# Optimization experiments

Measured on AMD Instinct MI355X. Metric: run time of the kernel, lower is better.

The kernel has to match this reference:

```python
import jax, jax.numpy as jnp
import numpy as np

H = 16      # numHeads (== numKeyValueHeads since keyValueHeadsPerHead=1)
D = 128     # headDim


def setup_inputs() -> dict:
    key = jax.random.key(0)
    k1, k2, k3 = jax.random.split(key, 3)
    B, S, dim = 2, 2048, 2048
    x = jax.random.normal(k1, (B, S, dim), dtype=jnp.float32)
    # qkvProj: Linear(dim -> (H + 2*H)*D) without bias; torch Linear weight is [out, in]
    Wqkv = jax.random.normal(k2, ((H + 2 * H) * D, dim), dtype=jnp.float32) * 0.02
    # outProj: Linear(H*D -> dim) without bias
    Wout = jax.random.normal(k3, (dim, H * D), dtype=jnp.float32) * 0.02
    return {"x": x, "Wqkv": Wqkv, "Wout": Wout}


def reference(x, Wqkv, Wout):
    B, S, _ = x.shape
    qkv = jnp.einsum('bsd,ed->bse', x, Wqkv)           # [B, S, 3*H*D]
    qkv = qkv.reshape(B, S, 3 * H, D)
    q = qkv[:, :, :H]                                  # [B, S, H, D]
    k = qkv[:, :, H:2 * H]                             # [B, S, H, D]
    v = qkv[:, :, 2 * H:]                              # [B, S, H, D]
    # explicit QK^T / sqrt(d), softmax in fp32, then @ V (keyValueHeadsPerHead=1
    # collapses the group axis, leaving standard per-head attention)
    logits = jnp.einsum('bqhd,bkhd->bhqk', q, k) * (D ** -0.5)
    w = jax.nn.softmax(logits.astype(jnp.float32), axis=-1).astype(logits.dtype)
    out = jnp.einsum('bhqk,bkhd->bqhd', w, v).reshape(B, S, H * D)
    return jnp.einsum('bse,de->bsd', out, Wout)        # outProj
```

## Files before the change

kernel.cpp:

```cpp
#include <hip/hip_runtime.h>

typedef __bf16 bf16x8 __attribute__((ext_vector_type(8)));
typedef _Float16 f16;
typedef f16 f16x8 __attribute__((ext_vector_type(8)));
typedef float f32x4 __attribute__((ext_vector_type(4)));
typedef unsigned short u16;
typedef u16 u16x4 __attribute__((ext_vector_type(4)));

__device__ __forceinline__ u16 f2bf(float f) {
  unsigned u = __builtin_bit_cast(unsigned, f);
  u += 0x7FFFu + ((u >> 16) & 1u);
  return (u16)(u >> 16);
}

#define GLDS16(g, l) __builtin_amdgcn_global_load_lds(                     \
    (const __attribute__((address_space(1))) unsigned int*)(g),            \
    (__attribute__((address_space(3))) unsigned int*)(l), 16, 0, 0)

__device__ __forceinline__ f32x4 mfma16(bf16x8 a, bf16x8 b, f32x4 c) {
  return __builtin_amdgcn_mfma_f32_16x16x32_bf16(a, b, c, 0, 0, 0);
}
__device__ __forceinline__ f32x4 mfma16h(f16x8 a, f16x8 b, f32x4 c) {
  return __builtin_amdgcn_mfma_f32_16x16x32_f16(a, b, c, 0, 0, 0);
}

__global__ void cvt_all(const float* __restrict__ x, const float* __restrict__ wqkv,
                        const float* __restrict__ wout, u16* __restrict__ xb,
                        u16* __restrict__ wqkvb, u16* __restrict__ woutb, float qscale) {
  int idx = blockIdx.x * blockDim.x + threadIdx.x;
  int stride = gridDim.x * blockDim.x;
  for (int i = idx; i < 6291456; i += stride) {
    const float* src; u16* dst; int j; float sc = 1.0f;
    if (i < 2097152)      { src = x;    dst = xb;    j = i; }
    else if (i < 5242880) { j = i - 2097152; src = wqkv; dst = wqkvb;
                            if (j < 1048576) sc = qscale; }
    else                  { j = i - 5242880; src = wout; dst = woutb; }
    float4 v = ((const float4*)src)[j];
    u16x4 o = { f2bf(v.x * sc), f2bf(v.y * sc), f2bf(v.z * sc), f2bf(v.w * sc) };
    ((u16x4*)dst)[j] = o;
  }
}

__global__ __launch_bounds__(512, 1) void gemm1_qkv(
    const u16* __restrict__ A, const u16* __restrict__ B,
    u16* __restrict__ QK, u16* __restrict__ VT) {
  __shared__ __align__(16) u16 LA[2][16384];
  __shared__ __align__(16) u16 LB[2][16384];
  constexpr int K = 2048;
  const int t = threadIdx.x, lane = t & 63, w = t >> 6;
  const int wm = w >> 2, wn = w & 3;
  const int l15 = lane & 15, lg = lane >> 4;
  const int l7 = l15 & 7;

  const int bid = blockIdx.x;
  const int wg = (bid & 7) * 48 + (bid >> 3);
  const int bx = wg % 24, by = wg / 24;
  const int m0 = by * 256, n0 = bx * 256;

  const int srow = t >> 3;
  const int schunk = (t & 7) ^ (srow & 7);
  const u16* ga = A + (size_t)(m0 + srow) * K + schunk * 8;
  const u16* gb = B + (size_t)(n0 + srow) * K + schunk * 8;

  f32x4 acc[8][4] = {};

#define SA(c, kt, d) GLDS16(ga + (kt) * 64 + (size_t)(c) * 64 * K, &LA[d][(c) * 4096] + t * 8)
#define SB(c, kt, d) GLDS16(gb + (kt) * 64 + (size_t)(c) * 64 * K, &LB[d][(c) * 4096] + t * 8)
#define BAR() __builtin_amdgcn_s_barrier()
#define LGKM0() asm volatile("s_waitcnt lgkmcnt(0)" ::: "memory")

  SA(0, 0, 0); SA(2, 0, 0); SB(0, 0, 0); SB(1, 0, 0); SB(2, 0, 0); SB(3, 0, 0);
  SA(1, 0, 0); SA(3, 0, 0);
  SA(0, 1, 1); SA(2, 1, 1); SB(0, 1, 1); SB(1, 1, 1); SB(2, 1, 1); SB(3, 1, 1);
  asm volatile("s_waitcnt vmcnt(6)" ::: "memory");
  BAR();

#pragma unroll 1
  for (int T = 0; T < 16; ++T) {
    const int k0 = 2 * T, k1 = 2 * T + 1;
    const bool st = (T < 15);
    bf16x8 aLo[2][4], aHi[2][4], bLo[2][2], bHi[2][2];

#pragma unroll
    for (int kk = 0; kk < 2; ++kk) {
      const int cp = ((kk * 4 + lg) ^ l7) * 8;
#pragma unroll
      for (int i = 0; i < 4; ++i)
        aLo[kk][i] = *(const bf16x8*)&LA[0][(wm * 128 + i * 16 + l15) * 64 + cp];
#pragma unroll
      for (int j = 0; j < 2; ++j)
        bLo[kk][j] = *(const bf16x8*)&LB[0][(wn * 64 + j * 16 + l15) * 64 + cp];
    }
    SA(1, k1, 1); SA(3, k1, 1);
    asm volatile("s_waitcnt lgkmcnt(8)" ::: "memory");
    BAR(); LGKM0();
    __builtin_amdgcn_s_setprio(1);
#pragma unroll
    for (int i = 0; i < 4; ++i)
#pragma unroll
      for (int j = 0; j < 2; ++j)
#pragma unroll
        for (int kk = 0; kk < 2; ++kk)
          acc[i][j] = mfma16(aLo[kk][i], bLo[kk][j], acc[i][j]);
    __builtin_amdgcn_s_setprio(0);
    BAR();

#pragma unroll
    for (int kk = 0; kk < 2; ++kk) {
      const int cp = ((kk * 4 + lg) ^ l7) * 8;
#pragma unroll
      for (int j = 0; j < 2; ++j)
        bHi[kk][j] = *(const bf16x8*)&LB[0][(wn * 64 + 32 + j * 16 + l15) * 64 + cp];
    }
    if (st) { SA(0, k0 + 2, 0); SA(2, k0 + 2, 0); }
    BAR(); LGKM0();
    __builtin_amdgcn_s_setprio(1);
#pragma unroll
    for (int i = 0; i < 4; ++i)
#pragma unroll
      for (int j = 0; j < 2; ++j)
#pragma unroll
        for (int kk = 0; kk < 2; ++kk)
          acc[i][2 + j] = mfma16(aLo[kk][i], bHi[kk][j], acc[i][2 + j]);
    __builtin_amdgcn_s_setprio(0);
    BAR();

#pragma unroll
    for (int kk = 0; kk < 2; ++kk) {
      const int cp = ((kk * 4 + lg) ^ l7) * 8;
#pragma unroll
      for (int i = 0; i < 4; ++i)
        aHi[kk][i] = *(const bf16x8*)&LA[0][(wm * 128 + 64 + i * 16 + l15) * 64 + cp];
    }
    if (st) { SB(0, k0 + 2, 0); SB(1, k0 + 2, 0); }
    BAR(); LGKM0();
    __builtin_amdgcn_s_setprio(1);
#pragma unroll
    for (int i = 0; i < 4; ++i)
#pragma unroll
      for (int j = 0; j < 2; ++j)
#pragma unroll
        for (int kk = 0; kk < 2; ++kk)
          acc[4 + i][j] = mfma16(aHi[kk][i], bLo[kk][j], acc[4 + i][j]);
    __builtin_amdgcn_s_setprio(0);
    BAR();

    if (st) {
      SB(2, k0 + 2, 0); SB(3, k0 + 2, 0);
      asm volatile("s_waitcnt vmcnt(6)" ::: "memory");
    } else {
      asm volatile("s_waitcnt vmcnt(0)" ::: "memory");
    }
    BAR();
    __builtin_amdgcn_s_setprio(1);
#pragma unroll
    for (int i = 0; i < 4; ++i)
#pragma unroll
      for (int j = 0; j < 2; ++j)
#pragma unroll
        for (int kk = 0; kk < 2; ++kk)
          acc[4 + i][2 + j] = mfma16(aHi[kk][i], bHi[kk][j], acc[4 + i][2 + j]);
    __builtin_amdgcn_s_setprio(0);
    BAR();

#pragma unroll
    for (int kk = 0; kk < 2; ++kk) {
      const int cp = ((kk * 4 + lg) ^ l7) * 8;
#pragma unroll
      for (int i = 0; i < 4; ++i)
        aLo[kk][i] = *(const bf16x8*)&LA[1][(wm * 128 + i * 16 + l15) * 64 + cp];
#pragma unroll
      for (int j = 0; j < 2; ++j)
        bLo[kk][j] = *(const bf16x8*)&LB[1][(wn * 64 + j * 16 + l15) * 64 + cp];
    }
    if (st) { SA(1, k0 + 2, 0); SA(3, k0 + 2, 0); }
    asm volatile("s_waitcnt lgkmcnt(8)" ::: "memory");
    BAR(); LGKM0();
    __builtin_amdgcn_s_setprio(1);
#pragma unroll
    for (int i = 0; i < 4; ++i)
#pragma unroll
      for (int j = 0; j < 2; ++j)
#pragma unroll
        for (int kk = 0; kk < 2; ++kk)
          acc[i][j] = mfma16(aLo[kk][i], bLo[kk][j], acc[i][j]);
    __builtin_amdgcn_s_setprio(0);
    BAR();

#pragma unroll
    for (int kk = 0; kk < 2; ++kk) {
      const int cp = ((kk * 4 + lg) ^ l7) * 8;
#pragma unroll
      for (int j = 0; j < 2; ++j)
        bHi[kk][j] = *(const bf16x8*)&LB[1][(wn * 64 + 32 + j * 16 + l15) * 64 + cp];
    }
    if (st) { SA(0, k1 + 2, 1); SA(2, k1 + 2, 1); }
    BAR(); LGKM0();
    __builtin_amdgcn_s_setprio(1);
#pragma unroll
    for (int i = 0; i < 4; ++i)
#pragma unroll
      for (int j = 0; j < 2; ++j)
#pragma unroll
        for (int kk = 0; kk < 2; ++kk)
          acc[i][2 + j] = mfma16(aLo[kk][i], bHi[kk][j], acc[i][2 + j]);
    __builtin_amdgcn_s_setprio(0);
    BAR();

#pragma unroll
    for (int kk = 0; kk < 2; ++kk) {
      const int cp = ((kk * 4 + lg) ^ l7) * 8;
#pragma unroll
      for (int i = 0; i < 4; ++i)
        aHi[kk][i] = *(const bf16x8*)&LA[1][(wm * 128 + 64 + i * 16 + l15) * 64 + cp];
    }
    if (st) { SB(0, k1 + 2, 1); SB(1, k1 + 2, 1); }
    BAR(); LGKM0();
    __builtin_amdgcn_s_setprio(1);
#pragma unroll
    for (int i = 0; i < 4; ++i)
#pragma unroll
      for (int j = 0; j < 2; ++j)
#pragma unroll
        for (int kk = 0; kk < 2; ++kk)
          acc[4 + i][j] = mfma16(aHi[kk][i], bLo[kk][j], acc[4 + i][j]);
    __builtin_amdgcn_s_setprio(0);
    BAR();

    if (st) {
      SB(2, k1 + 2, 1); SB(3, k1 + 2, 1);
      asm volatile("s_waitcnt vmcnt(6)" ::: "memory");
    }
    BAR();
    __builtin_amdgcn_s_setprio(1);
#pragma unroll
    for (int i = 0; i < 4; ++i)
#pragma unroll
      for (int j = 0; j < 2; ++j)
#pragma unroll
        for (int kk = 0; kk < 2; ++kk)
          acc[4 + i][2 + j] = mfma16(aHi[kk][i], bHi[kk][j], acc[4 + i][2 + j]);
    __builtin_amdgcn_s_setprio(0);
    BAR();
  }
#undef SA
#undef SB
#undef BAR
#undef LGKM0

  const int rb = m0 + wm * 128 + lg * 4;
  const int cb0 = wn * 64 + l15;
  if (n0 < 4096) {
#pragma unroll
    for (int i = 0; i < 8; ++i)
#pragma unroll
      for (int j = 0; j < 4; ++j) {
        const int row0 = rb + i * 16;
        const int col = n0 + cb0 + j * 16;
#pragma unroll
        for (int jj = 0; jj < 4; ++jj)
          QK[(size_t)(row0 + jj) * 4096 + col] = f2bf(acc[i][j][jj]);
      }
  } else {
#pragma unroll
    for (int i = 0; i < 8; ++i)
#pragma unroll
      for (int j = 0; j < 4; ++j) {
        const int row0 = rb + i * 16;
        const int vcol = (n0 - 4096) + cb0 + j * 16;
        const int bb = row0 >> 11, s = row0 & 2047;
        auto h0 = __builtin_amdgcn_cvt_pkrtz(acc[i][j][0], acc[i][j][1]);
        auto h1 = __builtin_amdgcn_cvt_pkrtz(acc[i][j][2], acc[i][j][3]);
        uint2 pk;
        pk.x = __builtin_bit_cast(unsigned, h0);
        pk.y = __builtin_bit_cast(unsigned, h1);
        *(uint2*)&VT[((size_t)bb * 2048 + vcol) * 2048 + s] = pk;
      }
  }
}

__global__ __launch_bounds__(256, 2) void gemm2_out(
    const u16* __restrict__ A, const u16* __restrict__ B,
    float* __restrict__ C) {
  __shared__ __align__(16) u16 LA[2][8192];
  __shared__ __align__(16) u16 LB[2][8192];
  constexpr int K = 2048, N = 2048;
  const int t = threadIdx.x, lane = t & 63, w = t >> 6;
  const int wm = w >> 1, wn = w & 1;
  const int l15 = lane & 15, lg = lane >> 4;
  const int l7 = l15 & 7;

  const int bid = blockIdx.x;
  const int wg = (bid & 7) * 64 + (bid >> 3);
  const int bx = wg & 15, by = wg >> 4;
  const int m0 = by * 128, n0 = bx * 128;

  const int srow = t >> 3;
  const int schunk = (t & 7) ^ (srow & 7);
  const u16* ga = A + (size_t)(m0 + srow) * K + schunk * 8;
  const u16* gb = B + (size_t)(n0 + srow) * K + schunk * 8;

  f32x4 acc[4][4] = {};

#define STG_A(ch, kt, bfi)                                                 \
    GLDS16(ga + (kt) * 64 + (size_t)(ch) * 32 * K, &LA[bfi][(ch) * 2048] + t * 8)
#define STG_B(ch, kt, bfi)                                                 \
    GLDS16(gb + (kt) * 64 + (size_t)(ch) * 32 * K, &LB[bfi][(ch) * 2048] + t * 8)
#define STG_ALL(kt, bfi) do {                                              \
    STG_A(0, kt, bfi); STG_A(1, kt, bfi); STG_A(2, kt, bfi); STG_A(3, kt, bfi); \
    STG_B(0, kt, bfi); STG_B(1, kt, bfi); STG_B(2, kt, bfi); STG_B(3, kt, bfi); \
  } while (0)

  STG_ALL(0, 0);

#pragma unroll 1
  for (int T = 0; T < 32; ++T) {
    const int p = T & 1, np = p ^ 1;
    if (T < 31) {
      STG_ALL(T + 1, np);
      asm volatile("s_waitcnt vmcnt(8)" ::: "memory");
    } else {
      asm volatile("s_waitcnt vmcnt(0)" ::: "memory");
    }
    __builtin_amdgcn_s_barrier();

    const u16* la = &LA[p][0];
    const u16* lb = &LB[p][0];
    bf16x8 aLo[2][2], aHi[2][2], bLo[2][2], bHi[2][2];
#pragma unroll
    for (int kk = 0; kk < 2; ++kk) {
      const int cp = ((kk * 4 + lg) ^ l7) * 8;
#pragma unroll
      for (int i = 0; i < 2; ++i) {
        aLo[kk][i] = *(const bf16x8*)&la[(wm * 64 + i * 16 + l15) * 64 + cp];
        bLo[kk][i] = *(const bf16x8*)&lb[(wn * 64 + i * 16 + l15) * 64 + cp];
        bHi[kk][i] = *(const bf16x8*)&lb[(wn * 64 + 32 + i * 16 + l15) * 64 + cp];
        aHi[kk][i] = *(const bf16x8*)&la[(wm * 64 + 32 + i * 16 + l15) * 64 + cp];
      }
    }
#pragma unroll
    for (int i = 0; i < 2; ++i)
#pragma unroll
      for (int j = 0; j < 2; ++j)
#pragma unroll
        for (int kk = 0; kk < 2; ++kk)
          acc[i][j] = mfma16(aLo[kk][i], bLo[kk][j], acc[i][j]);
#pragma unroll
    for (int i = 0; i < 2; ++i)
#pragma unroll
      for (int j = 0; j < 2; ++j)
#pragma unroll
        for (int kk = 0; kk < 2; ++kk)
          acc[i][2 + j] = mfma16(aLo[kk][i], bHi[kk][j], acc[i][2 + j]);
#pragma unroll
    for (int i = 0; i < 2; ++i)
#pragma unroll
      for (int j = 0; j < 2; ++j)
#pragma unroll
        for (int kk = 0; kk < 2; ++kk)
          acc[2 + i][j] = mfma16(aHi[kk][i], bLo[kk][j], acc[2 + i][j]);
#pragma unroll
    for (int i = 0; i < 2; ++i)
#pragma unroll
      for (int j = 0; j < 2; ++j)
#pragma unroll
        for (int kk = 0; kk < 2; ++kk)
          acc[2 + i][2 + j] = mfma16(aHi[kk][i], bHi[kk][j], acc[2 + i][2 + j]);

    asm volatile("s_waitcnt lgkmcnt(0)" ::: "memory");
    __builtin_amdgcn_s_barrier();
  }
#undef STG_A
#undef STG_B
#undef STG_ALL

  const int rb = m0 + wm * 64 + lg * 4;
  const int cb = n0 + wn * 64 + l15;
#pragma unroll
  for (int i = 0; i < 4; ++i)
#pragma unroll
    for (int j = 0; j < 4; ++j) {
      const int row0 = rb + i * 16;
      const int col = cb + j * 16;
#pragma unroll
      for (int jj = 0; jj < 4; ++jj)
        C[(size_t)(row0 + jj) * N + col] = acc[i][j][jj];
    }
}

#define PSTRIDE 72
__global__ __launch_bounds__(512, 1) void attn_fwd(
    const u16* __restrict__ qk, const u16* __restrict__ vt, u16* __restrict__ aout) {
  __shared__ __align__(16) u16 Ks[2][64 * 128];
  __shared__ __align__(16) u16 Vs[2][128 * 64];
  __shared__ __align__(16) u16 Pl[8][32 * PSTRIDE];
  const int t = threadIdx.x, lane = t & 63, w = t >> 6;
  const int bh = blockIdx.x;
  const int b = bh >> 4, h = bh & 15;
  const int q0 = blockIdx.y * 256 + w * 32;
  const int l15 = lane & 15, lg = lane >> 4;

  const u16* qp = qk + (size_t)b * 2048 * 4096 + h * 128;
  const u16* kp = qp + 2048;
  const u16* vtp = vt + (size_t)(b * 16 + h) * 128 * 2048;
  u16* op = aout + (size_t)b * 2048 * 2048 + h * 128;

  int ksoff[2], vsoff[2];
#pragma unroll
  for (int rd = 0; rd < 2; ++rd) {
    const int r = rd * 32 + (t >> 4);
    const int c = (t & 15) ^ (r & 15);
    ksoff[rd] = r * 4096 + c * 8;
    const int rv = rd * 64 + (t >> 3);
    const int cv = (t & 7) ^ (rv & 7);
    vsoff[rd] = rv * 2048 + cv * 8;
  }

  bf16x8 qf[2][4];
#pragma unroll
  for (int mi = 0; mi < 2; ++mi)
#pragma unroll
    for (int kd = 0; kd < 4; ++kd)
      qf[mi][kd] = *(const bf16x8*)&qp[(size_t)(q0 + mi * 16 + l15) * 4096 + kd * 32 + lg * 8];

  f32x4 o[2][8] = {};
  f32x4 lacc[2] = {};
  const f16x8 onesf = {f16(1.f), f16(1.f), f16(1.f), f16(1.f),
                       f16(1.f), f16(1.f), f16(1.f), f16(1.f)};
  u16* pw = &Pl[w][0];

#pragma unroll
  for (int rd = 0; rd < 2; ++rd) {
    GLDS16(kp + ksoff[rd], &Ks[0][0] + rd * 4096 + t * 8);
    GLDS16(vtp + vsoff[rd], &Vs[0][0] + rd * 4096 + t * 8);
  }
  __syncthreads();

  auto tile = [&](const u16* ksb, const u16* vsb, u16* kpre, u16* vpre, int nextit) {
    if (nextit < 32) {
      const size_t kt1 = (size_t)nextit * 64;
#pragma unroll
      for (int rd = 0; rd < 2; ++rd) {
        GLDS16(kp + kt1 * 4096 + ksoff[rd], kpre + rd * 4096 + t * 8);
        GLDS16(vtp + kt1 + vsoff[rd], vpre + rd * 4096 + t * 8);
      }
    }
    f32x4 sf[2][4];
    __builtin_amdgcn_s_setprio(1);
#pragma unroll
    for (int ni = 0; ni < 4; ++ni) {
      const int r = ni * 16 + l15;
      bf16x8 kf[4];
#pragma unroll
      for (int kd = 0; kd < 4; ++kd)
        kf[kd] = *(const bf16x8*)&ksb[r * 128 + (((kd * 4 + lg) ^ l15) * 8)];
#pragma unroll
      for (int mi = 0; mi < 2; ++mi) {
        f32x4 s = {0.f, 0.f, 0.f, 0.f};
        s = mfma16(kf[0], qf[mi][0], s);
        s = mfma16(kf[1], qf[mi][1], s);
        s = mfma16(kf[2], qf[mi][2], s);
        s = mfma16(kf[3], qf[mi][3], s);
        sf[mi][ni] = s;
      }
    }
    __builtin_amdgcn_s_setprio(0);

#pragma unroll
    for (int mi = 0; mi < 2; ++mi)
#pragma unroll
      for (int ni = 0; ni < 4; ++ni) {
        float p0 = exp2f(sf[mi][ni][0]);
        float p1 = exp2f(sf[mi][ni][1]);
        float p2 = exp2f(sf[mi][ni][2]);
        float p3 = exp2f(sf[mi][ni][3]);
        auto h0 = __builtin_amdgcn_cvt_pkrtz(p0, p1);
        auto h1 = __builtin_amdgcn_cvt_pkrtz(p2, p3);
        uint2 wv;
        wv.x = __builtin_bit_cast(unsigned, h0);
        wv.y = __builtin_bit_cast(unsigned, h1);
        *(uint2*)&pw[(mi * 16 + l15) * PSTRIDE + ni * 16 + lg * 4] = wv;
      }

    f16x8 pa[2][2];
#pragma unroll
    for (int mi = 0; mi < 2; ++mi)
#pragma unroll
      for (int ks = 0; ks < 2; ++ks)
        pa[mi][ks] = *(const f16x8*)&pw[(mi * 16 + l15) * PSTRIDE + ks * 32 + lg * 8];
    __builtin_amdgcn_s_setprio(1);
#pragma unroll
    for (int mi = 0; mi < 2; ++mi) {
      lacc[mi] = mfma16h(pa[mi][0], onesf, lacc[mi]);
      lacc[mi] = mfma16h(pa[mi][1], onesf, lacc[mi]);
    }
#pragma unroll
    for (int n2 = 0; n2 < 8; ++n2) {
      const int r = n2 * 16 + l15;
      f16x8 vf0 = *(const f16x8*)&vsb[r * 64 + (((0 * 4 + lg) ^ (l15 & 7)) * 8)];
      f16x8 vf1 = *(const f16x8*)&vsb[r * 64 + (((1 * 4 + lg) ^ (l15 & 7)) * 8)];
#pragma unroll
      for (int mi = 0; mi < 2; ++mi) {
        o[mi][n2] = mfma16h(pa[mi][0], vf0, o[mi][n2]);
        o[mi][n2] = mfma16h(pa[mi][1], vf1, o[mi][n2]);
      }
    }
    __builtin_amdgcn_s_setprio(0);
    __syncthreads();
  };

#pragma unroll 1
  for (int it = 0; it < 32; it += 2) {
    tile(&Ks[0][0], &Vs[0][0], &Ks[1][0], &Vs[1][0], it + 1);
    tile(&Ks[1][0], &Vs[1][0], &Ks[0][0], &Vs[0][0], it + 2);
  }

#pragma unroll
  for (int mi = 0; mi < 2; ++mi)
#pragma unroll
    for (int j = 0; j < 4; ++j) {
      float inv = 1.f / lacc[mi][j];
#pragma unroll
      for (int n2 = 0; n2 < 8; ++n2)
        op[(size_t)(q0 + mi * 16 + lg * 4 + j) * 2048 + n2 * 16 + l15] =
            f2bf(o[mi][n2][j] * inv);
    }
}

extern "C" void kernel_launch(void* const* d_in, const int* in_sizes, int n_in,
                              void* d_out, int out_size, void* d_ws, size_t ws_size,
                              hipStream_t stream) {
  const float* x    = (const float*)d_in[0];
  const float* Wqkv = (const float*)d_in[1];
  const float* Wout = (const float*)d_in[2];
  float* out = (float*)d_out;

  u16* ws = (u16*)d_ws;
  u16* xb    = ws;
  u16* wqkvb = ws + 8388608;
  u16* woutb = ws + 20971520;
  u16* qkbuf = ws + 25165824;
  u16* vtbuf = ws + 41943040;
  u16* aout  = xb;

  const float qscale = 0.08838834764831845f * 1.4426950408889634f;

  cvt_all<<<2048, 256, 0, stream>>>(x, Wqkv, Wout, xb, wqkvb, woutb, qscale);

  gemm1_qkv<<<384, 512, 0, stream>>>(xb, wqkvb, qkbuf, vtbuf);
  attn_fwd<<<dim3(32, 8, 1), 512, 0, stream>>>(qkbuf, vtbuf, aout);
  gemm2_out<<<512, 256, 0, stream>>>(aout, woutb, out);
}
```

Measured before the change: 256.2 us.

## Split QKV projection into separate QK and V GEMM kernels

The fused QKV GEMM (384 blocks of 256x256 tiles) is split into a QK GEMM with 256 blocks of 256x256 and a separate V GEMM with 512 blocks of 128x128 tiles that writes the transposed fp16 V. This gives each kernel a grid of 256 blocks that matches the CU count, so there is no partial second wave, and removes the branch in the epilogue. The cost is an extra kernel launch and lower data reuse for the V part. It also raises wave priority (s_setprio) around the MFMA sections in the V GEMM and the out-projection GEMM.

```diff
diff --git a/kernel.cpp b/kernel.cpp
--- a/kernel.cpp
+++ b/kernel.cpp
@@ -41,9 +41,9 @@
   }
 }
 
-__global__ __launch_bounds__(512, 1) void gemm1_qkv(
+__global__ __launch_bounds__(512, 1) void gemm1_qk(
     const u16* __restrict__ A, const u16* __restrict__ B,
-    u16* __restrict__ QK, u16* __restrict__ VT) {
+    u16* __restrict__ QK) {
   __shared__ __align__(16) u16 LA[2][16384];
   __shared__ __align__(16) u16 LB[2][16384];
   constexpr int K = 2048;
@@ -53,8 +53,8 @@
   const int l7 = l15 & 7;
 
   const int bid = blockIdx.x;
-  const int wg = (bid & 7) * 48 + (bid >> 3);
-  const int bx = wg % 24, by = wg / 24;
+  const int wg = (bid & 7) * 32 + (bid >> 3);
+  const int bx = wg & 15, by = wg >> 4;
   const int m0 = by * 256, n0 = bx * 256;
 
   const int srow = t >> 3;
@@ -249,34 +249,132 @@
 #undef LGKM0
 
   const int rb = m0 + wm * 128 + lg * 4;
-  const int cb0 = wn * 64 + l15;
-  if (n0 < 4096) {
-#pragma unroll
-    for (int i = 0; i < 8; ++i)
-#pragma unroll
-      for (int j = 0; j < 4; ++j) {
-        const int row0 = rb + i * 16;
-        const int col = n0 + cb0 + j * 16;
-#pragma unroll
-        for (int jj = 0; jj < 4; ++jj)
-          QK[(size_t)(row0 + jj) * 4096 + col] = f2bf(acc[i][j][jj]);
+  const int cb0 = n0 + wn * 64 + l15;
+#pragma unroll
+  for (int i = 0; i < 8; ++i)
+#pragma unroll
+    for (int j = 0; j < 4; ++j) {
+      const int row0 = rb + i * 16;
+      const int col = cb0 + j * 16;
+#pragma unroll
+      for (int jj = 0; jj < 4; ++jj)
+        QK[(size_t)(row0 + jj) * 4096 + col] = f2bf(acc[i][j][jj]);
+    }
+}
+
+__global__ __launch_bounds__(256, 2) void gemm1_v(
+    const u16* __restrict__ A, const u16* __restrict__ B,
+    u16* __restrict__ VT) {
+  __shared__ __align__(16) u16 LA[2][8192];
+  __shared__ __align__(16) u16 LB[2][8192];
+  constexpr int K = 2048;
+  const int t = threadIdx.x, lane = t & 63, w = t >> 6;
+  const int wm = w >> 1, wn = w & 1;
+  const int l15 = lane & 15, lg = lane >> 4;
+  const int l7 = l15 & 7;
+
+  const int bid = blockIdx.x;
+  const int wg = (bid & 7) * 64 + (bid >> 3);
+  const int bx = wg & 15, by = wg >> 4;
+  const int m0 = by * 128, n0 = bx * 128;
+
+  const int srow = t >> 3;
+  const int schunk = (t & 7) ^ (srow & 7);
+  const u16* ga = A + (size_t)(m0 + srow) * K + schunk * 8;
+  const u16* gb = B + (size_t)(n0 + srow) * K + schunk * 8;
+
+  f32x4 acc[4][4] = {};
+
+#define STG_A(ch, kt, bfi)                                                 \
+    GLDS16(ga + (kt) * 64 + (size_t)(ch) * 32 * K, &LA[bfi][(ch) * 2048] + t * 8)
+#define STG_B(ch, kt, bfi)                                                 \
+    GLDS16(gb + (kt) * 64 + (size_t)(ch) * 32 * K, &LB[bfi][(ch) * 2048] + t * 8)
+#define STG_ALL(kt, bfi) do {                                              \
+    STG_A(0, kt, bfi); STG_A(1, kt, bfi); STG_A(2, kt, bfi); STG_A(3, kt, bfi); \
+    STG_B(0, kt, bfi); STG_B(1, kt, bfi); STG_B(2, kt, bfi); STG_B(3, kt, bfi); \
+  } while (0)
+
+  STG_ALL(0, 0);
+
+#pragma unroll 1
+  for (int T = 0; T < 32; ++T) {
+    const int p = T & 1, np = p ^ 1;
+    if (T < 31) {
+      STG_ALL(T + 1, np);
+      asm volatile("s_waitcnt vmcnt(8)" ::: "memory");
+    } else {
+      asm volatile("s_waitcnt vmcnt(0)" ::: "memory");
+    }
+    __builtin_amdgcn_s_barrier();
+
+    const u16* la = &LA[p][0];
+    const u16* lb = &LB[p][0];
+    bf16x8 aLo[2][2], aHi[2][2], bLo[2][2], bHi[2][2];
+#pragma unroll
+    for (int kk = 0; kk < 2; ++kk) {
+      const int cp = ((kk * 4 + lg) ^ l7) * 8;
+#pragma unroll
+      for (int i = 0; i < 2; ++i) {
+        aLo[kk][i] = *(const bf16x8*)&la[(wm * 64 + i * 16 + l15) * 64 + cp];
+        bLo[kk][i] = *(const bf16x8*)&lb[(wn * 64 + i * 16 + l15) * 64 + cp];
+        bHi[kk][i] = *(const bf16x8*)&lb[(wn * 64 + 32 + i * 16 + l15) * 64 + cp];
+        aHi[kk][i] = *(const bf16x8*)&la[(wm * 64 + 32 + i * 16 + l15) * 64 + cp];
       }
-  } else {
-#pragma unroll
-    for (int i = 0; i < 8; ++i)
-#pragma unroll
-      for (int j = 0; j < 4; ++j) {
-        const int row0 = rb + i * 16;
-        const int vcol = (n0 - 4096) + cb0 + j * 16;
-        const int bb = row0 >> 11, s = row0 & 2047;
-        auto h0 = __builtin_amdgcn_cvt_pkrtz(acc[i][j][0], acc[i][j][1]);
-        auto h1 = __builtin_amdgcn_cvt_pkrtz(acc[i][j][2], acc[i][j][3]);
-        uint2 pk;
-        pk.x = __builtin_bit_cast(unsigned, h0);
-        pk.y = __builtin_bit_cast(unsigned, h1);
-        *(uint2*)&VT[((size_t)bb * 2048 + vcol) * 2048 + s] = pk;
-      }
+    }
+    __builtin_amdgcn_s_setprio(1);
+#pragma unroll
+    for (int i = 0; i < 2; ++i)
+#pragma unroll
+      for (int j = 0; j < 2; ++j)
+#pragma unroll
+        for (int kk = 0; kk < 2; ++kk)
+          acc[i][j] = mfma16(aLo[kk][i], bLo[kk][j], acc[i][j]);
+#pragma unroll
+    for (int i = 0; i < 2; ++i)
+#pragma unroll
+      for (int j = 0; j < 2; ++j)
+#pragma unroll
+        for (int kk = 0; kk < 2; ++kk)
+          acc[i][2 + j] = mfma16(aLo[kk][i], bHi[kk][j], acc[i][2 + j]);
+#pragma unroll
+    for (int i = 0; i < 2; ++i)
+#pragma unroll
+      for (int j = 0; j < 2; ++j)
+#pragma unroll
+        for (int kk = 0; kk < 2; ++kk)
+          acc[2 + i][j] = mfma16(aHi[kk][i], bLo[kk][j], acc[2 + i][j]);
+#pragma unroll
+    for (int i = 0; i < 2; ++i)
+#pragma unroll
+      for (int j = 0; j < 2; ++j)
+#pragma unroll
+        for (int kk = 0; kk < 2; ++kk)
+          acc[2 + i][2 + j] = mfma16(aHi[kk][i], bHi[kk][j], acc[2 + i][2 + j]);
+    __builtin_amdgcn_s_setprio(0);
+
+    asm volatile("s_waitcnt lgkmcnt(0)" ::: "memory");
+    __builtin_amdgcn_s_barrier();
   }
+#undef STG_A
+#undef STG_B
+#undef STG_ALL
+
+  const int rb = m0 + wm * 64 + lg * 4;
+  const int cb = n0 + wn * 64 + l15;
+#pragma unroll
+  for (int i = 0; i < 4; ++i)
+#pragma unroll
+    for (int j = 0; j < 4; ++j) {
+      const int row0 = rb + i * 16;
+      const int vcol = cb + j * 16;
+      const int bb = row0 >> 11, s = row0 & 2047;
+      auto h0 = __builtin_amdgcn_cvt_pkrtz(acc[i][j][0], acc[i][j][1]);
+      auto h1 = __builtin_amdgcn_cvt_pkrtz(acc[i][j][2], acc[i][j][3]);
+      uint2 pk;
+      pk.x = __builtin_bit_cast(unsigned, h0);
+      pk.y = __builtin_bit_cast(unsigned, h1);
+      *(uint2*)&VT[((size_t)bb * 2048 + vcol) * 2048 + s] = pk;
+    }
 }
 
 __global__ __launch_bounds__(256, 2) void gemm2_out(
@@ -338,6 +436,7 @@
         aHi[kk][i] = *(const bf16x8*)&la[(wm * 64 + 32 + i * 16 + l15) * 64 + cp];
       }
     }
+    __builtin_amdgcn_s_setprio(1);
 #pragma unroll
     for (int i = 0; i < 2; ++i)
 #pragma unroll
@@ -366,6 +465,7 @@
 #pragma unroll
         for (int kk = 0; kk < 2; ++kk)
           acc[2 + i][2 + j] = mfma16(aHi[kk][i], bHi[kk][j], acc[2 + i][2 + j]);
+    __builtin_amdgcn_s_setprio(0);
 
     asm volatile("s_waitcnt lgkmcnt(0)" ::: "memory");
     __builtin_amdgcn_s_barrier();
@@ -547,7 +647,8 @@
 
   cvt_all<<<2048, 256, 0, stream>>>(x, Wqkv, Wout, xb, wqkvb, woutb, qscale);
 
-  gemm1_qkv<<<384, 512, 0, stream>>>(xb, wqkvb, qkbuf, vtbuf);
+  gemm1_qk<<<256, 512, 0, stream>>>(xb, wqkvb, qkbuf);
+  gemm1_v<<<512, 256, 0, stream>>>(xb, wqkvb + (size_t)4096 * 2048, vtbuf);
   attn_fwd<<<dim3(32, 8, 1), 512, 0, stream>>>(qkbuf, vtbuf, aout);
   gemm2_out<<<512, 256, 0, stream>>>(aout, woutb, out);
 }
```

After: 240.8 us (median of 2 runs). 6.0% less time.

## Split QKV GEMM into QK and V kernels with 256x128 tile GEMM template

Applied to the files above, without the earlier changes.

The fused QKV projection (384 blocks of 256x256, which does not fill the CUs in a whole number of waves) is split into a QK GEMM with 256 blocks of 256x256 and a separate V GEMM. The V GEMM uses a new templated 256x128-tile kernel with split A-fragment loads and interleaved prefetch. The same template replaces the 128x128 output-projection GEMM, giving 256 blocks of 512 threads. This aims at better wave quantization and higher MFMA density per LDS load, at the cost of an extra kernel launch and a second read of x.

```diff
diff --git a/kernel.cpp b/kernel.cpp
--- a/kernel.cpp
+++ b/kernel.cpp
@@ -41,9 +41,9 @@
   }
 }
 
-__global__ __launch_bounds__(512, 1) void gemm1_qkv(
+__global__ __launch_bounds__(512, 1) void gemm1_qk(
     const u16* __restrict__ A, const u16* __restrict__ B,
-    u16* __restrict__ QK, u16* __restrict__ VT) {
+    u16* __restrict__ QK) {
   __shared__ __align__(16) u16 LA[2][16384];
   __shared__ __align__(16) u16 LB[2][16384];
   constexpr int K = 2048;
@@ -53,8 +53,8 @@
   const int l7 = l15 & 7;
 
   const int bid = blockIdx.x;
-  const int wg = (bid & 7) * 48 + (bid >> 3);
-  const int bx = wg % 24, by = wg / 24;
+  const int wg = (bid & 7) * 32 + (bid >> 3);
+  const int bx = wg & 15, by = wg >> 4;
   const int m0 = by * 256, n0 = bx * 256;
 
   const int srow = t >> 3;
@@ -245,147 +245,140 @@
   }
 #undef SA
 #undef SB
-#undef BAR
-#undef LGKM0
 
   const int rb = m0 + wm * 128 + lg * 4;
-  const int cb0 = wn * 64 + l15;
-  if (n0 < 4096) {
-#pragma unroll
-    for (int i = 0; i < 8; ++i)
-#pragma unroll
-      for (int j = 0; j < 4; ++j) {
-        const int row0 = rb + i * 16;
-        const int col = n0 + cb0 + j * 16;
-#pragma unroll
-        for (int jj = 0; jj < 4; ++jj)
-          QK[(size_t)(row0 + jj) * 4096 + col] = f2bf(acc[i][j][jj]);
-      }
-  } else {
-#pragma unroll
-    for (int i = 0; i < 8; ++i)
-#pragma unroll
-      for (int j = 0; j < 4; ++j) {
-        const int row0 = rb + i * 16;
-        const int vcol = (n0 - 4096) + cb0 + j * 16;
+  const int cb0 = n0 + wn * 64 + l15;
+#pragma unroll
+  for (int i = 0; i < 8; ++i)
+#pragma unroll
+    for (int j = 0; j < 4; ++j) {
+      const int row0 = rb + i * 16;
+      const int col = cb0 + j * 16;
+#pragma unroll
+      for (int jj = 0; jj < 4; ++jj)
+        QK[(size_t)(row0 + jj) * 4096 + col] = f2bf(acc[i][j][jj]);
+    }
+}
+
+template<int MODE>
+__global__ __launch_bounds__(512, 1) void gemm_mk(
+    const u16* __restrict__ A, const u16* __restrict__ B, void* __restrict__ C) {
+  __shared__ __align__(16) u16 LA[2][16384];
+  __shared__ __align__(16) u16 LB[2][8192];
+  constexpr int K = 2048;
+  const int t = threadIdx.x, lane = t & 63, w = t >> 6;
+  const int wm = w >> 2, wn = w & 3;
+  const int l15 = lane & 15, lg = lane >> 4;
+  const int l7 = l15 & 7;
+
+  const int bid = blockIdx.x;
+  const int wg = (bid & 7) * 32 + (bid >> 3);
+  const int bx = wg & 15, by = wg >> 4;
+  const int m0 = by * 256, n0 = bx * 128;
+
+  const int srow = t >> 3;
+  const int schunk = (t & 7) ^ (srow & 7);
+  const u16* ga = A + (size_t)(m0 + srow) * K + schunk * 8;
+  const u16* gb = B + (size_t)(n0 + srow) * K + schunk * 8;
+
+  f32x4 acc[8][2] = {};
+
+#define SA(c, kt, d) GLDS16(ga + (kt) * 64 + (size_t)(c) * 64 * K, &LA[d][(c) * 4096] + t * 8)
+#define SB(c, kt, d) GLDS16(gb + (kt) * 64 + (size_t)(c) * 64 * K, &LB[d][(c) * 4096] + t * 8)
+
+  SA(0, 0, 0); SA(2, 0, 0); SB(0, 0, 0); SB(1, 0, 0);
+  SA(1, 0, 0); SA(3, 0, 0);
+  asm volatile("s_waitcnt vmcnt(2)" ::: "memory");
+  __builtin_amdgcn_s_barrier();
+
+#pragma unroll 1
+  for (int T = 0; T < 32; ++T) {
+    const int p = T & 1, np = p ^ 1;
+    const bool st = (T < 31);
+    bf16x8 aF[2][4], bF[2][2];
+
+#pragma unroll
+    for (int kk = 0; kk < 2; ++kk) {
+      const int cp = ((kk * 4 + lg) ^ l7) * 8;
+#pragma unroll
+      for (int i = 0; i < 4; ++i)
+        aF[kk][i] = *(const bf16x8*)&LA[p][(wm * 128 + i * 16 + l15) * 64 + cp];
+#pragma unroll
+      for (int j = 0; j < 2; ++j)
+        bF[kk][j] = *(const bf16x8*)&LB[p][(wn * 32 + j * 16 + l15) * 64 + cp];
+    }
+    if (st) {
+      SA(0, T + 1, np); SA(2, T + 1, np); SB(0, T + 1, np); SB(1, T + 1, np);
+      asm volatile("s_waitcnt vmcnt(4)" ::: "memory");
+    } else {
+      asm volatile("s_waitcnt vmcnt(0)" ::: "memory");
+    }
+    __builtin_amdgcn_s_barrier();
+    asm volatile("s_waitcnt lgkmcnt(0)" ::: "memory");
+    __builtin_amdgcn_sched_barrier(0);
+    __builtin_amdgcn_s_setprio(1);
+#pragma unroll
+    for (int i = 0; i < 4; ++i)
+#pragma unroll
+      for (int j = 0; j < 2; ++j)
+#pragma unroll
+        for (int kk = 0; kk < 2; ++kk)
+          acc[i][j] = mfma16(aF[kk][i], bF[kk][j], acc[i][j]);
+    __builtin_amdgcn_s_setprio(0);
+    __builtin_amdgcn_s_barrier();
+
+#pragma unroll
+    for (int kk = 0; kk < 2; ++kk) {
+      const int cp = ((kk * 4 + lg) ^ l7) * 8;
+#pragma unroll
+      for (int i = 0; i < 4; ++i)
+        aF[kk][i] = *(const bf16x8*)&LA[p][(wm * 128 + 64 + i * 16 + l15) * 64 + cp];
+    }
+    if (st) {
+      SA(1, T + 1, np); SA(3, T + 1, np);
+      asm volatile("s_waitcnt vmcnt(2)" ::: "memory");
+    }
+    __builtin_amdgcn_s_barrier();
+    asm volatile("s_waitcnt lgkmcnt(0)" ::: "memory");
+    __builtin_amdgcn_sched_barrier(0);
+    __builtin_amdgcn_s_setprio(1);
+#pragma unroll
+    for (int i = 0; i < 4; ++i)
+#pragma unroll
+      for (int j = 0; j < 2; ++j)
+#pragma unroll
+        for (int kk = 0; kk < 2; ++kk)
+          acc[4 + i][j] = mfma16(aF[kk][i], bF[kk][j], acc[4 + i][j]);
+    __builtin_amdgcn_s_setprio(0);
+    __builtin_amdgcn_s_barrier();
+  }
+#undef SA
+#undef SB
+
+  const int rb = m0 + wm * 128 + lg * 4;
+  const int cb = n0 + wn * 32 + l15;
+#pragma unroll
+  for (int i = 0; i < 8; ++i) {
+#pragma unroll
+    for (int j = 0; j < 2; ++j) {
+      const int row0 = rb + i * 16;
+      const int col = cb + j * 16;
+      if (MODE == 0) {
         const int bb = row0 >> 11, s = row0 & 2047;
         auto h0 = __builtin_amdgcn_cvt_pkrtz(acc[i][j][0], acc[i][j][1]);
         auto h1 = __builtin_amdgcn_cvt_pkrtz(acc[i][j][2], acc[i][j][3]);
         uint2 pk;
         pk.x = __builtin_bit_cast(unsigned, h0);
         pk.y = __builtin_bit_cast(unsigned, h1);
-        *(uint2*)&VT[((size_t)bb * 2048 + vcol) * 2048 + s] = pk;
+        *(uint2*)&((u16*)C)[((size_t)bb * 2048 + col) * 2048 + s] = pk;
+      } else {
+        float* cf = (float*)C;
+#pragma unroll
+        for (int jj = 0; jj < 4; ++jj)
+          cf[(size_t)(row0 + jj) * 2048 + col] = acc[i][j][jj];
       }
-  }
-}
-
-__global__ __launch_bounds__(256, 2) void gemm2_out(
-    const u16* __restrict__ A, const u16* __restrict__ B,
-    float* __restrict__ C) {
-  __shared__ __align__(16) u16 LA[2][8192];
-  __shared__ __align__(16) u16 LB[2][8192];
-  constexpr int K = 2048, N = 2048;
-  const int t = threadIdx.x, lane = t & 63, w = t >> 6;
-  const int wm = w >> 1, wn = w & 1;
-  const int l15 = lane & 15, lg = lane >> 4;
-  const int l7 = l15 & 7;
-
-  const int bid = blockIdx.x;
-  const int wg = (bid & 7) * 64 + (bid >> 3);
-  const int bx = wg & 15, by = wg >> 4;
-  const int m0 = by * 128, n0 = bx * 128;
-
-  const int srow = t >> 3;
-  const int schunk = (t & 7) ^ (srow & 7);
-  const u16* ga = A + (size_t)(m0 + srow) * K + schunk * 8;
-  const u16* gb = B + (size_t)(n0 + srow) * K + schunk * 8;
-
-  f32x4 acc[4][4] = {};
-
-#define STG_A(ch, kt, bfi)                                                 \
-    GLDS16(ga + (kt) * 64 + (size_t)(ch) * 32 * K, &LA[bfi][(ch) * 2048] + t * 8)
-#define STG_B(ch, kt, bfi)                                                 \
-    GLDS16(gb + (kt) * 64 + (size_t)(ch) * 32 * K, &LB[bfi][(ch) * 2048] + t * 8)
-#define STG_ALL(kt, bfi) do {                                              \
-    STG_A(0, kt, bfi); STG_A(1, kt, bfi); STG_A(2, kt, bfi); STG_A(3, kt, bfi); \
-    STG_B(0, kt, bfi); STG_B(1, kt, bfi); STG_B(2, kt, bfi); STG_B(3, kt, bfi); \
-  } while (0)
-
-  STG_ALL(0, 0);
-
-#pragma unroll 1
-  for (int T = 0; T < 32; ++T) {
-    const int p = T & 1, np = p ^ 1;
-    if (T < 31) {
-      STG_ALL(T + 1, np);
-      asm volatile("s_waitcnt vmcnt(8)" ::: "memory");
-    } else {
-      asm volatile("s_waitcnt vmcnt(0)" ::: "memory");
-    }
-    __builtin_amdgcn_s_barrier();
-
-    const u16* la = &LA[p][0];
-    const u16* lb = &LB[p][0];
-    bf16x8 aLo[2][2], aHi[2][2], bLo[2][2], bHi[2][2];
-#pragma unroll
-    for (int kk = 0; kk < 2; ++kk) {
-      const int cp = ((kk * 4 + lg) ^ l7) * 8;
-#pragma unroll
-      for (int i = 0; i < 2; ++i) {
-        aLo[kk][i] = *(const bf16x8*)&la[(wm * 64 + i * 16 + l15) * 64 + cp];
-        bLo[kk][i] = *(const bf16x8*)&lb[(wn * 64 + i * 16 + l15) * 64 + cp];
-        bHi[kk][i] = *(const bf16x8*)&lb[(wn * 64 + 32 + i * 16 + l15) * 64 + cp];
-        aHi[kk][i] = *(const bf16x8*)&la[(wm * 64 + 32 + i * 16 + l15) * 64 + cp];
-      }
-    }
-#pragma unroll
-    for (int i = 0; i < 2; ++i)
-#pragma unroll
-      for (int j = 0; j < 2; ++j)
-#pragma unroll
-        for (int kk = 0; kk < 2; ++kk)
-          acc[i][j] = mfma16(aLo[kk][i], bLo[kk][j], acc[i][j]);
-#pragma unroll
-    for (int i = 0; i < 2; ++i)
-#pragma unroll
-      for (int j = 0; j < 2; ++j)
-#pragma unroll
-        for (int kk = 0; kk < 2; ++kk)
-          acc[i][2 + j] = mfma16(aLo[kk][i], bHi[kk][j], acc[i][2 + j]);
-#pragma unroll
-    for (int i = 0; i < 2; ++i)
-#pragma unroll
-      for (int j = 0; j < 2; ++j)
-#pragma unroll
-        for (int kk = 0; kk < 2; ++kk)
-          acc[2 + i][j] = mfma16(aHi[kk][i], bLo[kk][j], acc[2 + i][j]);
-#pragma unroll
-    for (int i = 0; i < 2; ++i)
-#pragma unroll
-      for (int j = 0; j < 2; ++j)
-#pragma unroll
-        for (int kk = 0; kk < 2; ++kk)
-          acc[2 + i][2 + j] = mfma16(aHi[kk][i], bHi[kk][j], acc[2 + i][2 + j]);
-
-    asm volatile("s_waitcnt lgkmcnt(0)" ::: "memory");
-    __builtin_amdgcn_s_barrier();
-  }
-#undef STG_A
-#undef STG_B
-#undef STG_ALL
-
-  const int rb = m0 + wm * 64 + lg * 4;
-  const int cb = n0 + wn * 64 + l15;
-#pragma unroll
-  for (int i = 0; i < 4; ++i)
-#pragma unroll
-    for (int j = 0; j < 4; ++j) {
-      const int row0 = rb + i * 16;
-      const int col = cb + j * 16;
-#pragma unroll
-      for (int jj = 0; jj < 4; ++jj)
-        C[(size_t)(row0 + jj) * N + col] = acc[i][j][jj];
-    }
+    }
+  }
 }
 
 #define PSTRIDE 72
@@ -547,7 +540,8 @@
 
   cvt_all<<<2048, 256, 0, stream>>>(x, Wqkv, Wout, xb, wqkvb, woutb, qscale);
 
-  gemm1_qkv<<<384, 512, 0, stream>>>(xb, wqkvb, qkbuf, vtbuf);
+  gemm1_qk<<<256, 512, 0, stream>>>(xb, wqkvb, qkbuf);
+  gemm_mk<0><<<256, 512, 0, stream>>>(xb, wqkvb + (size_t)4096 * 2048, (void*)vtbuf);
   attn_fwd<<<dim3(32, 8, 1), 512, 0, stream>>>(qkbuf, vtbuf, aout);
-  gemm2_out<<<512, 256, 0, stream>>>(aout, woutb, out);
-}
+  gemm_mk<1><<<256, 512, 0, stream>>>(aout, woutb, (void*)out);
+}
```

New measurement: 243.5 us. 5.0% less time.
